# Performance work log

Measured on AMD Instinct MI355X. Metric: run time of the kernel, lower is better.

Reference implementation:

```python
import jax, jax.numpy as jnp
import numpy as np

N_SEG, B, COND = 16, 256, 512
H, OUT = 1024, 512


def setup_inputs() -> dict:
    key = jax.random.key(0)
    ks = jax.random.split(key, 14)
    s = 0.05  # keep gates in non-saturated range
    return {
        "c": jax.random.normal(ks[0], (N_SEG, B, COND), jnp.float32),
        "W_init": jax.random.normal(ks[1], (4 * H, COND), jnp.float32) * s,
        "b_init": jax.random.normal(ks[2], (4 * H,), jnp.float32) * s,
        "W_ih1": jax.random.normal(ks[3], (4 * H, COND + OUT), jnp.float32) * s,
        "W_hh1": jax.random.normal(ks[4], (4 * H, H), jnp.float32) * s,
        "b_ih1": jax.random.normal(ks[5], (4 * H,), jnp.float32) * s,
        "b_hh1": jax.random.normal(ks[6], (4 * H,), jnp.float32) * s,
        "W_ih2": jax.random.normal(ks[7], (4 * H, H), jnp.float32) * s,
        "W_hh2": jax.random.normal(ks[8], (4 * H, H), jnp.float32) * s,
        "b_ih2": jax.random.normal(ks[9], (4 * H,), jnp.float32) * s,
        "b_hh2": jax.random.normal(ks[10], (4 * H,), jnp.float32) * s,
        "W_out": jax.random.normal(ks[11], (OUT, H), jnp.float32) * s,
        "b_out": jax.random.normal(ks[12], (OUT,), jnp.float32) * s,
        "length": 32,
        "epoch": 10,
        "k": 200,
    }


def _lstm_cell(x, h, c, W_ih, W_hh, b_ih, b_hh):
    # PyTorch LSTMCell gate order: input, forget, cell, output
    g = x @ W_ih.T + b_ih + h @ W_hh.T + b_hh
    i, f, gg, o = jnp.split(g, 4, axis=-1)
    c_new = jax.nn.sigmoid(f) * c + jax.nn.sigmoid(i) * jnp.tanh(gg)
    h_new = jax.nn.sigmoid(o) * jnp.tanh(c_new)
    return h_new, c_new


def reference(c, W_init, b_init, W_ih1, W_hh1, b_ih1, b_hh1,
              W_ih2, W_hh2, b_ih2, b_hh2, W_out, b_out,
              length, epoch, k):
    steps = length // 2
    n_seg, bsz, _ = c.shape

    def segment(prev, embed):
        # fresh LSTM states from the conductor embedding
        t = jnp.tanh(embed @ W_init.T + b_init)  # [B, 4H]
        h1, h2, c1, c2 = jnp.split(t, 4, axis=-1)

        def step(carry, _):
            h1, c1, h2, c2, prev = carry
            prev = jax.lax.stop_gradient(prev)  # training=False path: detach
            x = jnp.concatenate([embed, prev], axis=1)  # [B, COND+OUT]
            h1n, c1n = _lstm_cell(x, h1, c1, W_ih1, W_hh1, b_ih1, b_hh1)
            h2n, c2n = _lstm_cell(h1n, h2, c2, W_ih2, W_hh2, b_ih2, b_hh2)
            out = h2n @ W_out.T + b_out  # [B, OUT]
            return (h1n, c1n, h2n, c2n, out), out

        (_, _, _, _, prev), outs = jax.lax.scan(
            step, (h1, h2_init := h2, c1, c2, prev)[:0] or (h1, c1, h2, c2, prev),
            None, length=steps)
        return prev, outs  # outs: [steps, B, OUT]

    prev0 = jnp.zeros((bsz, OUT), dtype=c.dtype)
    _, outs = jax.lax.scan(segment, prev0, c)  # [n_seg, steps, B, OUT]
    outputs = outs.reshape(n_seg * steps, bsz, OUT).transpose(1, 0, 2)
    ratio = jnp.float32(k / (k + np.exp(epoch / k)))
    return outputs, ratio
```

## Files before the change

kernel.cpp:

```cpp
#include <hip/hip_runtime.h>
#include <hip/hip_bf16.h>

using bf16 = __hip_bfloat16;
typedef __attribute__((ext_vector_type(8))) short bf16x8;
typedef __attribute__((ext_vector_type(4))) float f32x4;

__device__ __forceinline__ void gload16(const void* g, void* l) {
  __builtin_amdgcn_global_load_lds((const __attribute__((address_space(1))) void*)g,
                                   (__attribute__((address_space(3))) void*)l, 16, 0, 0);
}

__device__ __forceinline__ float sigm(float x) { return 1.0f / (1.0f + __expf(-x)); }
__device__ __forceinline__ float ftanh(float x) {
  float e = __expf(2.0f * fabsf(x));
  return copysignf(1.0f - 2.0f / (e + 1.0f), x);
}
__device__ __forceinline__ float bf2f(unsigned short u) {
  union { unsigned int i; float f; } v; v.i = (unsigned int)u << 16; return v.f;
}

#define MFMA16(a, b, c) __builtin_amdgcn_mfma_f32_16x16x32_bf16(a, b, c, 0, 0, 0)
#define WAITV(n) asm volatile("s_waitcnt vmcnt(" #n ")" ::: "memory")
#define BARRIER() do { __builtin_amdgcn_s_barrier(); asm volatile("" ::: "memory"); } while (0)

struct Frag { bf16x8 a0, a1, b0, b1; };

__global__ __launch_bounds__(512) void rnn_step(
    const bf16* __restrict__ a1, const bf16* __restrict__ a2,
    const bf16* __restrict__ w1, const bf16* __restrict__ w2,
    const bf16* __restrict__ pe, const float* __restrict__ bias,
    const float* __restrict__ bsub,
    const float* __restrict__ c_in, float* __restrict__ c_out,
    bf16* __restrict__ h_out, bf16* __restrict__ hrow_out)
{
  __shared__ __attribute__((aligned(128))) char smem[131072];
  const int tid = threadIdx.x;
  const int wv = tid >> 6, ln = tid & 63;
  const int grp = wv >> 2, wg = wv & 3;
  const int bid = blockIdx.x;
  const int nt = ((bid & 7) << 3) | ((bid >> 3) & 7);
  const int mt = bid >> 6;
  const int m0 = mt << 6, n0 = nt << 6;
  const int wm = (wg >> 1) << 5, wn = (wg & 1) << 5;
  const bool use2 = (a2 != nullptr);

  const bf16* asrc = (grp == 0) ? a1 : (use2 ? a2 : a1);
  const bf16* wsrc = (grp == 0) ? w1 : (use2 ? w2 : w1);
  char* gbase = smem + (grp << 16);

  const int srow = (wg << 4) + (ln >> 2);
  const int skc  = (ln & 3) ^ ((srow >> 1) & 3);
  const size_t aGOff = ((size_t)(m0 + srow) << 11) + (skc << 4);
  const size_t bGOff = ((size_t)(n0 + srow) << 11) + (skc << 4);

  auto stage = [&](int kb) {
    char* dst = gbase + ((kb & 7) << 13) + (wg << 10);
    gload16((const char*)asrc + aGOff + ((size_t)kb << 6), dst);
    gload16((const char*)wsrc + bGOff + ((size_t)kb << 6), dst + 4096);
  };

  const int kc = ln >> 4;
  const int ar0 = wm + (ln & 15), ar1 = ar0 + 16;
  const int br0 = wn + (ln & 15), br1 = br0 + 16;
  const int aoff0 = ar0 * 64 + ((kc ^ ((ar0 >> 1) & 3)) << 4);
  const int aoff1 = ar1 * 64 + ((kc ^ ((ar1 >> 1) & 3)) << 4);
  const int boff0 = 4096 + br0 * 64 + ((kc ^ ((br0 >> 1) & 3)) << 4);
  const int boff1 = 4096 + br1 * 64 + ((kc ^ ((br1 >> 1) & 3)) << 4);

  auto ldfrags = [&](int kb, Frag& f) {
    const char* base = gbase + ((kb & 7) << 13);
    f.a0 = *(const bf16x8*)(base + aoff0);
    f.a1 = *(const bf16x8*)(base + aoff1);
    f.b0 = *(const bf16x8*)(base + boff0);
    f.b1 = *(const bf16x8*)(base + boff1);
  };

  f32x4 acc00{}, acc01{}, acc10{}, acc11{};
  auto domfma = [&](Frag& f) {
    acc00 = MFMA16(f.a0, f.b0, acc00);
    acc01 = MFMA16(f.a0, f.b1, acc01);
    acc10 = MFMA16(f.a1, f.b0, acc10);
    acc11 = MFMA16(f.a1, f.b1, acc11);
  };

  Frag f0, f1;
  stage(0); stage(1); stage(2); stage(3); stage(4); stage(5);
  WAITV(8); BARRIER();
  ldfrags(0, f0); ldfrags(1, f1);
  stage(6); stage(7);
  __builtin_amdgcn_s_setprio(1);
  domfma(f0); domfma(f1);
  __builtin_amdgcn_s_setprio(0);
  for (int p = 1; p <= 13; ++p) {
    const int kb = p << 1;
    WAITV(8); BARRIER();
    ldfrags(kb, f0); ldfrags(kb + 1, f1);
    if (kb + 6 < 32) stage(kb + 6);
    if (kb + 7 < 32) stage(kb + 7);
    __builtin_amdgcn_s_setprio(1);
    domfma(f0); domfma(f1);
    __builtin_amdgcn_s_setprio(0);
  }
  WAITV(4); BARRIER();
  ldfrags(28, f0); ldfrags(29, f1);
  __builtin_amdgcn_s_setprio(1);
  domfma(f0); domfma(f1);
  __builtin_amdgcn_s_setprio(0);
  WAITV(0); BARRIER();
  ldfrags(30, f0); ldfrags(31, f1);
  __builtin_amdgcn_s_setprio(1);
  domfma(f0); domfma(f1);
  __builtin_amdgcn_s_setprio(0);

  __syncthreads();
  float* gs = (float*)smem;
#pragma unroll
  for (int mi = 0; mi < 2; ++mi)
#pragma unroll
    for (int ni = 0; ni < 2; ++ni) {
      f32x4 a = (mi == 0) ? (ni == 0 ? acc00 : acc01) : (ni == 0 ? acc10 : acc11);
#pragma unroll
      for (int r = 0; r < 4; ++r) {
        int row = wm + mi * 16 + ((ln >> 4) << 2) + r;
        int col = wn + ni * 16 + (ln & 15);
        gs[grp * 4352 + row * 68 + col] = a[r];
      }
    }
  __syncthreads();

  const int h = tid & 15, mr = tid >> 4;
  const int hg = (nt << 4) + h;
#pragma unroll
  for (int half = 0; half < 2; ++half) {
    int m = mr + (half << 5);
    int gm = m0 + m;
    float4 v = *(const float4*)(gs + m * 68 + (h << 2));
    float g0 = v.x, g1 = v.y, g2 = v.z, g3 = v.w;
    if (use2) {
      float4 u = *(const float4*)(gs + 4352 + m * 68 + (h << 2));
      g0 += u.x; g1 += u.y; g2 += u.z; g3 += u.w;
    }
    int nb = n0 + (h << 2);
    if (pe) {
      ushort4 pv = *(const ushort4*)((const unsigned short*)pe + (size_t)gm * 4096 + nb);
      g0 += bf2f(pv.x); g1 += bf2f(pv.y); g2 += bf2f(pv.z); g3 += bf2f(pv.w);
    }
    if (bias){ float4 bv = *(const float4*)(bias + nb);
              g0 += bv.x; g1 += bv.y; g2 += bv.z; g3 += bv.w; }
    if (bsub){ float4 sv = *(const float4*)(bsub + nb);
              g0 -= sv.x; g1 -= sv.y; g2 -= sv.z; g3 -= sv.w; }
    float ig = sigm(g0), fg = sigm(g1), gg = ftanh(g2), og = sigm(g3);
    size_t idx = (size_t)gm * 1024 + hg;
    float cn = fg * c_in[idx] + ig * gg;
    c_out[idx] = cn;
    bf16 hv = __float2bfloat16(og * ftanh(cn));
    h_out[idx] = hv;
    if (hrow_out) {
      unsigned short us = *(unsigned short*)&hv;
      __builtin_nontemporal_store(us, (unsigned short*)(hrow_out + idx));
    }
  }
}

template <int EP>
__global__ __launch_bounds__(256) void gemm_ep(
    const bf16* __restrict__ A, const bf16* __restrict__ W, int K,
    const float* __restrict__ bias,
    float* __restrict__ f1, float* __restrict__ f2,
    bf16* __restrict__ o1, bf16* __restrict__ o2, int gt_base)
{
  __shared__ __attribute__((aligned(128))) char smem[32768];
  const int tid = threadIdx.x;
  const int wv = tid >> 6, ln = tid & 63;
  const int n0 = blockIdx.x << 6;
  const int m0 = blockIdx.y << 6;
  const int Nn = (int)(gridDim.x << 6);
  const int wm = (wv >> 1) << 5, wn = (wv & 1) << 5;
  const int nkb = K >> 6;

  f32x4 acc00{}, acc01{}, acc10{}, acc11{};

  auto stage = [&](int kb, int buf) {
    int k0 = kb << 6;
    char* As = smem + buf * 16384;
    char* Bs = As + 8192;
#pragma unroll
    for (int i = 0; i < 2; ++i) {
      int r = ((i << 2) + wv) * 8 + (ln >> 3);
      int sc = (ln & 7) ^ (r & 7);
      gload16((const char*)(A + (size_t)(m0 + r) * K + k0) + (sc << 4),
              As + (((i << 2) + wv) << 10));
      gload16((const char*)(W + (size_t)(n0 + r) * K + k0) + (sc << 4),
              Bs + (((i << 2) + wv) << 10));
    }
  };

  stage(0, 0);
  __syncthreads();
  for (int kb = 0; kb < nkb; ++kb) {
    int buf = kb & 1;
    if (kb + 1 < nkb) stage(kb + 1, buf ^ 1);
    const char* As = smem + buf * 16384;
    const char* Bs = As + 8192;
#pragma unroll
    for (int ks = 0; ks < 2; ++ks) {
      const int kc = (ks << 2) + (ln >> 4);
      auto ld = [&](const char* base, int row) -> bf16x8 {
        return *(const bf16x8*)(base + row * 128 + ((kc ^ (row & 7)) << 4));
      };
      bf16x8 A0 = ld(As, wm + (ln & 15));
      bf16x8 A1 = ld(As, wm + 16 + (ln & 15));
      bf16x8 B0 = ld(Bs, wn + (ln & 15));
      bf16x8 B1 = ld(Bs, wn + 16 + (ln & 15));
      acc00 = MFMA16(A0, B0, acc00);
      acc01 = MFMA16(A0, B1, acc01);
      acc10 = MFMA16(A1, B0, acc10);
      acc11 = MFMA16(A1, B1, acc11);
    }
    __syncthreads();
  }

#pragma unroll
  for (int mi = 0; mi < 2; ++mi)
#pragma unroll
    for (int ni = 0; ni < 2; ++ni) {
      f32x4 a = (mi == 0) ? (ni == 0 ? acc00 : acc01) : (ni == 0 ? acc10 : acc11);
#pragma unroll
      for (int r = 0; r < 4; ++r) {
        int m = m0 + wm + mi * 16 + ((ln >> 4) << 2) + r;
        int n = n0 + wn + ni * 16 + (ln & 15);
        float v = a[r];
        if constexpr (EP == 0) {
          o1[(size_t)m * Nn + n] = __float2bfloat16(v);
        } else if constexpr (EP == 1) {
          v = tanhf(v + bias[n]);
          int q = n >> 10, hh = n & 1023;
          size_t idx = (size_t)m * 1024 + hh;
          if (q == 0)      o1[idx] = __float2bfloat16(v);
          else if (q == 1) o2[idx] = __float2bfloat16(v);
          else if (q == 2) f1[idx] = v;
          else             f2[idx] = v;
        } else if constexpr (EP == 2) {
          o1[(size_t)m * 4096 + n] = __float2bfloat16(v + bias[n]);
        } else {
          int b = m & 255, g = (m >> 8) + gt_base;
          f1[(size_t)b * 131072 + (size_t)g * 512 + n] = v + bias[n];
        }
      }
    }
}

__global__ void k_conv(const float* __restrict__ s, bf16* __restrict__ d, int n) {
  int i = blockIdx.x * 256 + threadIdx.x;
  if (i < n) d[i] = __float2bfloat16(s[i]);
}
__global__ void k_trans_wout(const float* __restrict__ s, bf16* __restrict__ d) {
  int i = blockIdx.x * 256 + threadIdx.x;
  int l = i >> 9, j = i & 511;
  d[i] = __float2bfloat16(s[(size_t)j * 1024 + l]);
}
__global__ void k_reorder_g(const float* __restrict__ s, bf16* __restrict__ d) {
  int i = blockIdx.x * 256 + threadIdx.x;
  int np = i >> 10, kx = i & 1023;
  int hh = np >> 2, q = np & 3;
  d[i] = __float2bfloat16(s[(size_t)(q * 1024 + hh) * 1024 + kx]);
}
__global__ void k_reorder_c(const float* __restrict__ s, bf16* __restrict__ d, int coloff) {
  int i = blockIdx.x * 256 + threadIdx.x;
  int np = i >> 9, kx = i & 511;
  int hh = np >> 2, q = np & 3;
  d[i] = __float2bfloat16(s[(size_t)(q * 1024 + hh) * 1024 + coloff + kx]);
}
__global__ void k_bias(const float* __restrict__ bih1, const float* __restrict__ bhh1,
                       const float* __restrict__ bih2, const float* __restrict__ bhh2,
                       const float* __restrict__ bo,   const float* __restrict__ Wih1,
                       float* __restrict__ b1r, float* __restrict__ b2r,
                       float* __restrict__ bfr) {
  int n = blockIdx.x * 256 + threadIdx.x;
  int hh = n >> 2, q = n & 3, r = q * 1024 + hh;
  const float* wrow = Wih1 + (size_t)r * 1024 + 512;
  float acc = 0.f;
  for (int j = 0; j < 512; ++j) acc += bo[j] * wrow[j];
  bfr[n] = acc;
  b1r[n] = bih1[r] + bhh1[r] + acc;
  b2r[n] = bih2[r] + bhh2[r];
}
__global__ void k_ratio(float* __restrict__ dst, const int* __restrict__ ep,
                        const int* __restrict__ kv) {
  float kf = (float)kv[0];
  dst[0] = kf / (kf + __expf((float)ep[0] / kf));
}

extern "C" void kernel_launch(void* const* d_in, const int* in_sizes, int n_in,
                              void* d_out, int out_size, void* d_ws, size_t ws_size,
                              hipStream_t stream) {
  (void)in_sizes; (void)n_in; (void)ws_size;
  const float* in_c     = (const float*)d_in[0];
  const float* in_Winit = (const float*)d_in[1];
  const float* in_binit = (const float*)d_in[2];
  const float* in_Wih1  = (const float*)d_in[3];
  const float* in_Whh1  = (const float*)d_in[4];
  const float* in_bih1  = (const float*)d_in[5];
  const float* in_bhh1  = (const float*)d_in[6];
  const float* in_Wih2  = (const float*)d_in[7];
  const float* in_Whh2  = (const float*)d_in[8];
  const float* in_bih2  = (const float*)d_in[9];
  const float* in_bhh2  = (const float*)d_in[10];
  const float* in_Wout  = (const float*)d_in[11];
  const float* in_bout  = (const float*)d_in[12];
  const int*   in_epoch = (const int*)d_in[14];
  const int*   in_k     = (const int*)d_in[15];
  float* out = (float*)d_out;

  char* p = (char*)d_ws;
  auto alloc = [&](size_t bytes) { char* q = p; p += (bytes + 255) & ~(size_t)255; return q; };
  bf16* wHH1  = (bf16*)alloc(4096ull * 1024 * 2);
  bf16* wFOLD = (bf16*)alloc(4096ull * 1024 * 2);
  bf16* wIH2  = (bf16*)alloc(4096ull * 1024 * 2);
  bf16* wHH2  = (bf16*)alloc(4096ull * 1024 * 2);
  bf16* wOUT  = (bf16*)alloc(512ull * 1024 * 2);
  bf16* wOUTT = (bf16*)alloc(1024ull * 512 * 2);
  bf16* wINIT = (bf16*)alloc(4096ull * 512 * 2);
  bf16* wIH1C = (bf16*)alloc(4096ull * 512 * 2);
  bf16* wPREV = (bf16*)alloc(4096ull * 512 * 2);
  bf16* cbf   = (bf16*)alloc(4096ull * 512 * 2);
  float* b1r  = (float*)alloc(4096 * 4);
  float* b2r  = (float*)alloc(4096 * 4);
  float* bfr  = (float*)alloc(4096 * 4);
  bf16* h1i   = (bf16*)alloc(16ull * 256 * 1024 * 2);
  bf16* h2i   = (bf16*)alloc(16ull * 256 * 1024 * 2);
  float* c1i  = (float*)alloc(16ull * 256 * 1024 * 4);
  float* c2i  = (float*)alloc(16ull * 256 * 1024 * 4);
  bf16* PE1   = (bf16*)alloc(16ull * 256 * 4096 * 2);
  bf16* h1b[2]; bf16* h2b[2]; float* c1b[2]; float* c2b[2];
  for (int i = 0; i < 2; ++i) {
    h1b[i] = (bf16*)alloc(256ull * 1024 * 2);
    h2b[i] = (bf16*)alloc(256ull * 1024 * 2);
    c1b[i] = (float*)alloc(256ull * 1024 * 4);
    c2b[i] = (float*)alloc(256ull * 1024 * 4);
  }
  bf16* hist = (bf16*)alloc(256ull * 256 * 1024 * 2);

  k_conv<<<8192, 256, 0, stream>>>(in_c, cbf, 2097152);
  k_conv<<<2048, 256, 0, stream>>>(in_Wout, wOUT, 524288);
  k_conv<<<8192, 256, 0, stream>>>(in_Winit, wINIT, 2097152);
  k_trans_wout<<<2048, 256, 0, stream>>>(in_Wout, wOUTT);
  k_reorder_g<<<16384, 256, 0, stream>>>(in_Whh1, wHH1);
  k_reorder_g<<<16384, 256, 0, stream>>>(in_Wih2, wIH2);
  k_reorder_g<<<16384, 256, 0, stream>>>(in_Whh2, wHH2);
  k_reorder_c<<<8192, 256, 0, stream>>>(in_Wih1, wIH1C, 0);
  k_reorder_c<<<8192, 256, 0, stream>>>(in_Wih1, wPREV, 512);
  k_bias<<<16, 256, 0, stream>>>(in_bih1, in_bhh1, in_bih2, in_bhh2, in_bout,
                                 in_Wih1, b1r, b2r, bfr);
  gemm_ep<0><<<dim3(16, 64), 256, 0, stream>>>(wPREV, wOUTT, 512, nullptr,
                                               nullptr, nullptr, wFOLD, nullptr, 0);
  gemm_ep<1><<<dim3(64, 64), 256, 0, stream>>>(cbf, wINIT, 512, in_binit,
                                               c1i, c2i, h1i, h2i, 0);
  gemm_ep<2><<<dim3(64, 64), 256, 0, stream>>>(cbf, wIH1C, 512, b1r,
                                               nullptr, nullptr, PE1, nullptr, 0);

  const size_t S = 256ull * 1024;
  for (int s = 0; s < 16; ++s) {
    for (int t = 0; t < 16; ++t) {
      int gt = s * 16 + t;
      int cur = gt & 1, prv = cur ^ 1;
      const bf16* h2prev = (gt == 0) ? nullptr : h2b[prv];
      rnn_step<<<256, 512, 0, stream>>>(
          (t == 0) ? h1i + (size_t)s * S : h1b[prv], h2prev,
          wHH1, wFOLD,
          PE1 + (size_t)s * 1048576, nullptr, (gt == 0) ? bfr : nullptr,
          (t == 0) ? c1i + (size_t)s * S : c1b[prv], c1b[cur],
          h1b[cur], nullptr);
      rnn_step<<<256, 512, 0, stream>>>(
          h1b[cur],
          (t == 0) ? h2i + (size_t)s * S : h2b[prv],
          wIH2, wHH2, nullptr, b2r, nullptr,
          (t == 0) ? c2i + (size_t)s * S : c2b[prv], c2b[cur],
          h2b[cur], hist + (size_t)gt * S);
    }
  }

  gemm_ep<3><<<dim3(8, 1024), 256, 0, stream>>>(hist, wOUT, 1024, in_bout,
                                                out, nullptr, nullptr, nullptr, 0);
  k_ratio<<<1, 1, 0, stream>>>(out + (out_size - 1), in_epoch, in_k);
}
```

Measured before the change: 6.164 ms.

## Deepen LDS ring to nine slots with three k-blocks per barrier and prefetch epilogue inputs

```diff
diff --git a/kernel.cpp b/kernel.cpp
--- a/kernel.cpp
+++ b/kernel.cpp
@@ -15,8 +15,8 @@
   float e = __expf(2.0f * fabsf(x));
   return copysignf(1.0f - 2.0f / (e + 1.0f), x);
 }
-__device__ __forceinline__ float bf2f(unsigned short u) {
-  union { unsigned int i; float f; } v; v.i = (unsigned int)u << 16; return v.f;
+__device__ __forceinline__ float bf2f(unsigned int u) {
+  union { unsigned int i; float f; } v; v.i = u << 16; return v.f;
 }
 
 #define MFMA16(a, b, c) __builtin_amdgcn_mfma_f32_16x16x32_bf16(a, b, c, 0, 0, 0)
@@ -33,7 +33,7 @@
     const float* __restrict__ c_in, float* __restrict__ c_out,
     bf16* __restrict__ h_out, bf16* __restrict__ hrow_out)
 {
-  __shared__ __attribute__((aligned(128))) char smem[131072];
+  __shared__ __attribute__((aligned(128))) char smem[147456];
   const int tid = threadIdx.x;
   const int wv = tid >> 6, ln = tid & 63;
   const int grp = wv >> 2, wg = wv & 3;
@@ -46,7 +46,19 @@
 
   const bf16* asrc = (grp == 0) ? a1 : (use2 ? a2 : a1);
   const bf16* wsrc = (grp == 0) ? w1 : (use2 ? w2 : w1);
-  char* gbase = smem + (grp << 16);
+  char* gbase = smem + grp * 73728;
+
+  const int eh = tid & 15, emr = tid >> 4;
+  const int ehg = (nt << 4) + eh;
+  const size_t eidx0 = (size_t)(m0 + emr) * 1024 + ehg;
+  const size_t eidx1 = (size_t)(m0 + emr + 32) * 1024 + ehg;
+  float c0 = c_in[eidx0], c1 = c_in[eidx1];
+  uint2 pv0 = make_uint2(0u, 0u), pv1 = make_uint2(0u, 0u);
+  if (pe) {
+    const unsigned short* peu = (const unsigned short*)pe;
+    pv0 = *(const uint2*)(peu + (size_t)(m0 + emr) * 4096 + n0 + (eh << 2));
+    pv1 = *(const uint2*)(peu + (size_t)(m0 + emr + 32) * 4096 + n0 + (eh << 2));
+  }
 
   const int srow = (wg << 4) + (ln >> 2);
   const int skc  = (ln & 3) ^ ((srow >> 1) & 3);
@@ -54,7 +66,7 @@
   const size_t bGOff = ((size_t)(n0 + srow) << 11) + (skc << 4);
 
   auto stage = [&](int kb) {
-    char* dst = gbase + ((kb & 7) << 13) + (wg << 10);
+    char* dst = gbase + (kb % 9) * 8192 + (wg << 10);
     gload16((const char*)asrc + aGOff + ((size_t)kb << 6), dst);
     gload16((const char*)wsrc + bGOff + ((size_t)kb << 6), dst + 4096);
   };
@@ -68,7 +80,7 @@
   const int boff1 = 4096 + br1 * 64 + ((kc ^ ((br1 >> 1) & 3)) << 4);
 
   auto ldfrags = [&](int kb, Frag& f) {
-    const char* base = gbase + ((kb & 7) << 13);
+    const char* base = gbase + (kb % 9) * 8192;
     f.a0 = *(const bf16x8*)(base + aoff0);
     f.a1 = *(const bf16x8*)(base + aoff1);
     f.b0 = *(const bf16x8*)(base + boff0);
@@ -83,29 +95,31 @@
     acc11 = MFMA16(f.a1, f.b1, acc11);
   };
 
-  Frag f0, f1;
+  Frag f0, f1, f2;
   stage(0); stage(1); stage(2); stage(3); stage(4); stage(5);
-  WAITV(8); BARRIER();
-  ldfrags(0, f0); ldfrags(1, f1);
-  stage(6); stage(7);
-  __builtin_amdgcn_s_setprio(1);
-  domfma(f0); domfma(f1);
-  __builtin_amdgcn_s_setprio(0);
-  for (int p = 1; p <= 13; ++p) {
-    const int kb = p << 1;
-    WAITV(8); BARRIER();
-    ldfrags(kb, f0); ldfrags(kb + 1, f1);
-    if (kb + 6 < 32) stage(kb + 6);
-    if (kb + 7 < 32) stage(kb + 7);
-    __builtin_amdgcn_s_setprio(1);
-    domfma(f0); domfma(f1);
-    __builtin_amdgcn_s_setprio(0);
-  }
-  WAITV(4); BARRIER();
-  ldfrags(28, f0); ldfrags(29, f1);
-  __builtin_amdgcn_s_setprio(1);
-  domfma(f0); domfma(f1);
-  __builtin_amdgcn_s_setprio(0);
+
+#define PHASE(K0, WN, S0, S1, S2, NS) do {                       \
+    WAITV(WN); BARRIER();                                        \
+    if ((NS) > 0) stage(S0);                                     \
+    if ((NS) > 1) stage(S1);                                     \
+    if ((NS) > 2) stage(S2);                                     \
+    ldfrags((K0), f0); ldfrags((K0) + 1, f1); ldfrags((K0) + 2, f2); \
+    __builtin_amdgcn_s_setprio(1);                               \
+    domfma(f0); domfma(f1); domfma(f2);                          \
+    __builtin_amdgcn_s_setprio(0);                               \
+  } while (0)
+
+  PHASE(0,  6,  6,  7,  8, 3);
+  PHASE(3,  6,  9, 10, 11, 3);
+  PHASE(6,  6, 12, 13, 14, 3);
+  PHASE(9,  6, 15, 16, 17, 3);
+  PHASE(12, 6, 18, 19, 20, 3);
+  PHASE(15, 6, 21, 22, 23, 3);
+  PHASE(18, 6, 24, 25, 26, 3);
+  PHASE(21, 6, 27, 28, 29, 3);
+  PHASE(24, 6, 30, 31,  0, 2);
+  PHASE(27, 4,  0,  0,  0, 0);
+#undef PHASE
   WAITV(0); BARRIER();
   ldfrags(30, f0); ldfrags(31, f1);
   __builtin_amdgcn_s_setprio(1);
@@ -128,30 +142,29 @@
     }
   __syncthreads();
 
-  const int h = tid & 15, mr = tid >> 4;
-  const int hg = (nt << 4) + h;
 #pragma unroll
   for (int half = 0; half < 2; ++half) {
-    int m = mr + (half << 5);
+    int m = emr + (half << 5);
     int gm = m0 + m;
-    float4 v = *(const float4*)(gs + m * 68 + (h << 2));
+    float4 v = *(const float4*)(gs + m * 68 + (eh << 2));
     float g0 = v.x, g1 = v.y, g2 = v.z, g3 = v.w;
     if (use2) {
-      float4 u = *(const float4*)(gs + 4352 + m * 68 + (h << 2));
+      float4 u = *(const float4*)(gs + 4352 + m * 68 + (eh << 2));
       g0 += u.x; g1 += u.y; g2 += u.z; g3 += u.w;
     }
-    int nb = n0 + (h << 2);
+    int nb = n0 + (eh << 2);
     if (pe) {
-      ushort4 pv = *(const ushort4*)((const unsigned short*)pe + (size_t)gm * 4096 + nb);
-      g0 += bf2f(pv.x); g1 += bf2f(pv.y); g2 += bf2f(pv.z); g3 += bf2f(pv.w);
+      uint2 pv = half ? pv1 : pv0;
+      g0 += bf2f(pv.x & 0xffffu); g1 += bf2f(pv.x >> 16);
+      g2 += bf2f(pv.y & 0xffffu); g3 += bf2f(pv.y >> 16);
     }
     if (bias){ float4 bv = *(const float4*)(bias + nb);
               g0 += bv.x; g1 += bv.y; g2 += bv.z; g3 += bv.w; }
     if (bsub){ float4 sv = *(const float4*)(bsub + nb);
               g0 -= sv.x; g1 -= sv.y; g2 -= sv.z; g3 -= sv.w; }
     float ig = sigm(g0), fg = sigm(g1), gg = ftanh(g2), og = sigm(g3);
-    size_t idx = (size_t)gm * 1024 + hg;
-    float cn = fg * c_in[idx] + ig * gg;
+    size_t idx = half ? eidx1 : eidx0;
+    float cn = fg * (half ? c1 : c0) + ig * gg;
     c_out[idx] = cn;
     bf16 hv = __float2bfloat16(og * ftanh(cn));
     h_out[idx] = hv;
```

New measurement: 6.219 ms. Within noise of the previous version (+0.9%).
